# Kernel optimization log

Measured on AMD Instinct MI355X. Metric: run time of the kernel, lower is better.

## Reference

```python
import jax, jax.numpy as jnp
import numpy as np

EPS = 1e-6


def setup_inputs() -> dict:
    key = jax.random.key(0)
    ks = jax.random.split(key, 7)
    b, n, d, H, hid = 4, 512, 128, 4, 32
    scale1 = 1.0 / np.sqrt(2 * d)
    scale2 = 1.0 / np.sqrt(hid)
    return {
        "x": jax.random.normal(ks[0], (b, n, d), dtype=jnp.float32),
        "W1": jax.random.normal(ks[1], (H, 2 * d, hid), dtype=jnp.float32) * scale1,
        "b1": jax.random.normal(ks[2], (H, hid), dtype=jnp.float32) * scale1,
        "W2": jax.random.normal(ks[3], (H, hid), dtype=jnp.float32) * scale2,
        "b2": jax.random.normal(ks[4], (H,), dtype=jnp.float32) * scale2,
        "Wp": jax.random.normal(ks[5], (d, d), dtype=jnp.float32) / np.sqrt(d),
        "bp": jax.random.normal(ks[6], (d,), dtype=jnp.float32) / np.sqrt(d),
    }


def reference(x, W1, b1, W2, b2, Wp, bp):
    # x: [b, n, d]; W1: [H, 2d, hid]; W2: [H, hid]
    d = x.shape[-1]
    # squared pairwise distance via gram matrix: ||xi - xj||^2
    sq = jnp.sum(x * x, axis=-1)                                   # [b, n]
    gram = jnp.einsum("bnd,bmd->bnm", x, x)                        # [b, n, n]
    dist2 = jnp.maximum(sq[:, :, None] + sq[:, None, :] - 2.0 * gram, 0.0)
    # per-head first linear on cat([xi, xj]) split into two projections
    ai = jnp.einsum("bnd,hdk->bhnk", x, W1[:, :d, :])              # [b, H, n, hid]
    aj = jnp.einsum("bnd,hdk->bhnk", x, W1[:, d:, :])              # [b, H, n, hid]
    pre = jnp.tanh(ai[:, :, :, None, :] + aj[:, :, None, :, :]
                   + b1[None, :, None, None, :])                   # [b, H, n, n, hid]
    sigma = jax.nn.softplus(jnp.einsum("bhnmk,hk->bhnm", pre, W2)
                            + b2[None, :, None, None])             # [b, H, n, n]
    adj = jnp.exp(-dist2[:, None, :, :] / (2.0 * sigma * sigma + EPS))
    adj_mean = jnp.mean(adj, axis=1)                               # [b, n, n]
    h = jnp.einsum("bnm,bmd->bnd", adj_mean, x)                    # [b, n, d]
    return h @ Wp + bp
```

## Files before the change

kernel.cpp:

```cpp
#include <hip/hip_runtime.h>

typedef float v4f __attribute__((ext_vector_type(4)));
typedef float v2f __attribute__((ext_vector_type(2)));

#define LOG2E  1.4426950408889634f
#define NLOG2E (-1.4426950408889634f)
#define C2L2E  2.8853900817779268f
#define LN2    0.6931471805599453f

__device__ __forceinline__ float fexp2(float x){ return __builtin_amdgcn_exp2f(x); }
__device__ __forceinline__ float flog2(float x){ return __builtin_amdgcn_logf(x); }
__device__ __forceinline__ float frcp (float x){ return __builtin_amdgcn_rcpf(x); }
__device__ __forceinline__ float hsum(v4f v){ return (v.x+v.y)+(v.z+v.w); }

__global__ __launch_bounds__(256) void prep_kernel(
    const float* __restrict__ x, const float* __restrict__ W1,
    const float* __restrict__ b1, const float* __restrict__ Wp,
    float* __restrict__ sq, float* __restrict__ Abuf,
    float* __restrict__ Bbuf, float* __restrict__ xpT)
{
  const int bid = blockIdx.x, t = threadIdx.x;
  if (bid >= 192) {
    int row = (bid - 192) * 256 + t;
    const v4f* xv = (const v4f*)(x + row * 128);
    float s = 0.f;
#pragma unroll
    for (int q = 0; q < 32; q++) { v4f v = xv[q]; s += hsum(v * v); }
    sq[row] = s;
    return;
  }
  __shared__ v4f Xs[64 * 9];
  __shared__ v4f Ws[32 * 16];
  const bool isAB = bid < 128;
  int it, ct;
  if (isAB) { it = bid >> 2; ct = bid & 3; }
  else      { int q = bid - 128; it = q >> 1; ct = q & 1; }
  const int row0 = it * 64;
  const int tx = t & 15, ty = t >> 4;
  const int r0 = ty * 4, c0 = tx * 4;
  v4f acc[4] = {};

  for (int dd0 = 0; dd0 < 128; dd0 += 32) {
    __syncthreads();
#pragma unroll
    for (int s2 = 0; s2 < 2; s2++) {
      int idx = t + s2 * 256;
      int row = idx >> 3, k4 = idx & 7;
      v4f v = *(const v4f*)(x + (row0 + row) * 128 + dd0 + k4 * 4);
      Xs[row * 9 + ((k4 + (row >> 2)) & 7)] = v;
    }
#pragma unroll
    for (int s2 = 0; s2 < 2; s2++) {
      int idx = t + s2 * 256;
      int dd = idx >> 4, cf4 = idx & 15;
      v4f v;
      if (isAB) {
        int cl = cf4 * 4; int half = cl >> 5; int k = cl & 31;
        v = *(const v4f*)(W1 + (ct * 256 + half * 128 + dd0 + dd) * 32 + k);
      } else {
        v = *(const v4f*)(Wp + (dd0 + dd) * 128 + ct * 64 + cf4 * 4);
      }
      Ws[dd * 16 + cf4] = v;
    }
    __syncthreads();
#pragma unroll
    for (int dd4 = 0; dd4 < 8; dd4++) {
      int sa = (dd4 + ty) & 7;
      v4f a0 = Xs[(r0 + 0) * 9 + sa], a1 = Xs[(r0 + 1) * 9 + sa];
      v4f a2 = Xs[(r0 + 2) * 9 + sa], a3 = Xs[(r0 + 3) * 9 + sa];
#pragma unroll
      for (int u = 0; u < 4; u++) {
        v4f bv = Ws[(dd4 * 4 + u) * 16 + tx];
        acc[0] += a0[u] * bv; acc[1] += a1[u] * bv;
        acc[2] += a2[u] * bv; acc[3] += a3[u] * bv;
      }
    }
  }

  if (isAB) {
    const int h = ct; const int half = c0 >> 5; const int k = c0 & 31;
    v4f bias = {};
    if (half == 0) bias = *(const v4f*)(b1 + h * 32 + k);
    float* dst = (half == 0) ? Abuf : Bbuf;
#pragma unroll
    for (int i = 0; i < 4; i++) {
      int rg = row0 + r0 + i; int b = rg >> 9; int ir = rg & 511;
      v4f o = (acc[i] + bias) * C2L2E;
      *(v4f*)(dst + ((b * 4 + h) * 512 + ir) * 32 + k) = o;
    }
  } else {
    int rg0 = row0 + r0; int b = rg0 >> 9; int ir0 = rg0 & 511;
#pragma unroll
    for (int u = 0; u < 4; u++) {
      int c = ct * 64 + c0 + u;
      v4f o = { acc[0][u], acc[1][u], acc[2][u], acc[3][u] };
      *(v4f*)(xpT + (b * 128 + c) * 512 + ir0) = o;
    }
  }
}

__global__ __launch_bounds__(256) void dist2_kernel(
    const float* __restrict__ x, const float* __restrict__ sq,
    float* __restrict__ D2)
{
  const int jt = blockIdx.x, it = blockIdx.y, b = blockIdx.z;
  const int t = threadIdx.x, tx = t & 15, ty = t >> 4;
  const int r0 = 2 * ty, c0 = 2 * tx;
  __shared__ v4f Xis[32 * 9], Xjs[32 * 9];
  const float* xb = x + b * 512 * 128;
  v4f acc[4] = {};
  const int row = t >> 3, k4l = t & 7, slot = (k4l + (row >> 1)) & 7;

  for (int dd0 = 0; dd0 < 128; dd0 += 32) {
    __syncthreads();
    Xis[row * 9 + slot] = *(const v4f*)(xb + (it * 32 + row) * 128 + dd0 + k4l * 4);
    Xjs[row * 9 + slot] = *(const v4f*)(xb + (jt * 32 + row) * 128 + dd0 + k4l * 4);
    __syncthreads();
#pragma unroll
    for (int k4 = 0; k4 < 8; k4++) {
      int sa = (k4 + ty) & 7, sb = (k4 + tx) & 7;
      v4f a0 = Xis[(r0 + 0) * 9 + sa], a1 = Xis[(r0 + 1) * 9 + sa];
      v4f b0 = Xjs[(c0 + 0) * 9 + sb], b1v = Xjs[(c0 + 1) * 9 + sb];
      acc[0] += a0 * b0; acc[1] += a0 * b1v;
      acc[2] += a1 * b0; acc[3] += a1 * b1v;
    }
  }
  float si0 = sq[b * 512 + it * 32 + r0], si1 = sq[b * 512 + it * 32 + r0 + 1];
  float sj0 = sq[b * 512 + jt * 32 + c0], sj1 = sq[b * 512 + jt * 32 + c0 + 1];
  v2f d0 = { fmaxf(si0 + sj0 - 2.f * hsum(acc[0]), 0.f),
             fmaxf(si0 + sj1 - 2.f * hsum(acc[1]), 0.f) };
  v2f d1 = { fmaxf(si1 + sj0 - 2.f * hsum(acc[2]), 0.f),
             fmaxf(si1 + sj1 - 2.f * hsum(acc[3]), 0.f) };
  float* dst = D2 + ((size_t)(b * 512 + it * 32 + r0)) * 512 + jt * 32 + c0;
  *(v2f*)dst = d0;
  *(v2f*)(dst + 512) = d1;
}

__global__ __launch_bounds__(256) void adj_kernel(
    const float* __restrict__ Abuf, const float* __restrict__ Bbuf,
    const float* __restrict__ W2, const float* __restrict__ b2g,
    const float* __restrict__ D2, float* __restrict__ ADJ)
{
  const int jt = blockIdx.x, it = blockIdx.y, b = blockIdx.z;
  const int t = threadIdx.x, tx = t & 15, ty = t >> 4;
  const int r0 = 2 * ty, c0 = 2 * tx;
  __shared__ v4f As[32 * 9], Bs[32 * 9];
  __shared__ v4f W2s[32];
  __shared__ float hb[4];

  if (t < 32) W2s[t] = ((const v4f*)W2)[t];
  if (t < 4) {
    float s = b2g[t];
    for (int k = 0; k < 32; k++) s += W2[t * 32 + k];
    hb[t] = s;
  }

  const float* d2p = D2 + ((size_t)(b * 512 + it * 32 + r0)) * 512 + jt * 32 + c0;
  v2f d2a = *(const v2f*)d2p;
  v2f d2b = *(const v2f*)(d2p + 512);
  float d2L[4] = { d2a.x * NLOG2E, d2a.y * NLOG2E, d2b.x * NLOG2E, d2b.y * NLOG2E };

  const int row = t >> 3, k4l = t & 7, slot = (k4l + (row >> 1)) & 7;
  float accA[4] = {0.f, 0.f, 0.f, 0.f};

  v4f pa = *(const v4f*)(Abuf + ((size_t)((b * 4 + 0) * 512 + it * 32 + row)) * 32 + k4l * 4);
  v4f pb = *(const v4f*)(Bbuf + ((size_t)((b * 4 + 0) * 512 + jt * 32 + row)) * 32 + k4l * 4);

  for (int h = 0; h < 4; h++) {
    __syncthreads();
    As[row * 9 + slot] = pa;
    Bs[row * 9 + slot] = pb;
    __syncthreads();
    if (h < 3) {
      pa = *(const v4f*)(Abuf + ((size_t)((b * 4 + h + 1) * 512 + it * 32 + row)) * 32 + k4l * 4);
      pb = *(const v4f*)(Bbuf + ((size_t)((b * 4 + h + 1) * 512 + jt * 32 + row)) * 32 + k4l * 4);
    }
    float hbv = hb[h];
    float sacc[4] = { hbv, hbv, hbv, hbv };
#pragma unroll
    for (int k4 = 0; k4 < 8; k4++) {
      int sa = (k4 + ty) & 7, sb = (k4 + tx) & 7;
      v4f a0 = As[(r0 + 0) * 9 + sa], a1 = As[(r0 + 1) * 9 + sa];
      v4f b0 = Bs[(c0 + 0) * 9 + sb], b1v = Bs[(c0 + 1) * 9 + sb];
      v4f w2v = W2s[h * 8 + k4];
#pragma unroll
      for (int u = 0; u < 4; u++) {
        float wm = -2.f * w2v[u];
        float a0u = a0[u], a1u = a1[u], b0u = b0[u], b1u = b1v[u];
        float e;
        e = fexp2(a0u + b0u); sacc[0] = fmaf(wm, frcp(e + 1.f), sacc[0]);
        e = fexp2(a0u + b1u); sacc[1] = fmaf(wm, frcp(e + 1.f), sacc[1]);
        e = fexp2(a1u + b0u); sacc[2] = fmaf(wm, frcp(e + 1.f), sacc[2]);
        e = fexp2(a1u + b1u); sacc[3] = fmaf(wm, frcp(e + 1.f), sacc[3]);
      }
    }
#pragma unroll
    for (int p = 0; p < 4; p++) {
      float u2 = fexp2(sacc[p] * LOG2E);
      float sg = LN2 * flog2(1.f + u2);
      float den = fmaf(2.f * sg, sg, 1e-6f);
      accA[p] += fexp2(d2L[p] * frcp(den));
    }
  }
  float* dst = ADJ + ((size_t)(b * 512 + it * 32 + r0)) * 512 + jt * 32 + c0;
  v2f o0 = { accA[0] * 0.25f, accA[1] * 0.25f };
  v2f o1 = { accA[2] * 0.25f, accA[3] * 0.25f };
  *(v2f*)dst = o0;
  *(v2f*)(dst + 512) = o1;
}

__global__ __launch_bounds__(256) void out_gemm(
    const float* __restrict__ ADJ, const float* __restrict__ xpT,
    float* __restrict__ part)
{
  const int ct = blockIdx.x;
  const int it = blockIdx.y;
  const int z = blockIdx.z; const int b = z >> 2, ks = z & 3;
  const int t = threadIdx.x, tx = t & 15, ty = t >> 4;
  const int r0 = 2 * ty, c0 = 2 * tx;
  __shared__ v4f Ajs[32 * 9], Xps[32 * 9];
  v4f acc[4] = {};
  const int row = t >> 3, k4l = t & 7, slot = (k4l + (row >> 1)) & 7;

  for (int k0 = ks * 128; k0 < ks * 128 + 128; k0 += 32) {
    __syncthreads();
    Ajs[row * 9 + slot] = *(const v4f*)(ADJ + ((size_t)(b * 512 + it * 32 + row)) * 512 + k0 + k4l * 4);
    Xps[row * 9 + slot] = *(const v4f*)(xpT + ((size_t)(b * 128 + ct * 32 + row)) * 512 + k0 + k4l * 4);
    __syncthreads();
#pragma unroll
    for (int k4 = 0; k4 < 8; k4++) {
      int sa = (k4 + ty) & 7, sb = (k4 + tx) & 7;
      v4f a0 = Ajs[(r0 + 0) * 9 + sa], a1 = Ajs[(r0 + 1) * 9 + sa];
      v4f b0 = Xps[(c0 + 0) * 9 + sb], b1v = Xps[(c0 + 1) * 9 + sb];
      acc[0] += a0 * b0; acc[1] += a0 * b1v;
      acc[2] += a1 * b0; acc[3] += a1 * b1v;
    }
  }
  float* dst = part + ((size_t)((ks * 4 + b) * 512 + it * 32 + r0)) * 128 + ct * 32 + c0;
  v2f o0 = { hsum(acc[0]), hsum(acc[1]) };
  v2f o1 = { hsum(acc[2]), hsum(acc[3]) };
  *(v2f*)dst = o0;
  *(v2f*)(dst + 128) = o1;
}

__global__ __launch_bounds__(256) void reduce_out(
    const float* __restrict__ part, const float* __restrict__ bp,
    float* __restrict__ out)
{
  int g = blockIdx.x * 256 + threadIdx.x;
  const v4f* p = (const v4f*)part;
  v4f s = p[g] + p[g + 65536] + p[g + 131072] + p[g + 196608];
  v4f bv = ((const v4f*)bp)[g & 31];
  ((v4f*)out)[g] = s + bv;
}

extern "C" void kernel_launch(void* const* d_in, const int* in_sizes, int n_in,
                              void* d_out, int out_size, void* d_ws, size_t ws_size,
                              hipStream_t stream) {
  const float* x  = (const float*)d_in[0];
  const float* W1 = (const float*)d_in[1];
  const float* b1 = (const float*)d_in[2];
  const float* W2 = (const float*)d_in[3];
  const float* b2 = (const float*)d_in[4];
  const float* Wp = (const float*)d_in[5];
  const float* bp = (const float*)d_in[6];
  float* out = (float*)d_out;

  float* ws  = (float*)d_ws;
  float* sq  = ws;
  float* A   = ws + 2048;
  float* Bb  = A + 262144;
  float* xpT = Bb + 262144;
  float* D2  = xpT + 262144;
  float* ADJ = D2 + 1048576;
  float* part = D2;

  prep_kernel<<<200, 256, 0, stream>>>(x, W1, b1, Wp, sq, A, Bb, xpT);
  dist2_kernel<<<dim3(16, 16, 4), 256, 0, stream>>>(x, sq, D2);
  adj_kernel<<<dim3(16, 16, 4), 256, 0, stream>>>(A, Bb, W2, b2, D2, ADJ);
  out_gemm<<<dim3(4, 16, 16), 256, 0, stream>>>(ADJ, xpT, part);
  reduce_out<<<256, 256, 0, stream>>>(part, bp, out);
}
```

Measured before the change: 68.32 us.

## Fuse distance computation into adjacency kernel and drop split-K output reduction

Moves the Gram-matrix distance computation into the adjacency kernel, reusing its shared-memory tiles, so the D2 matrix is never written to or read back from global memory and one launch disappears. It also replaces the split-K output GEMM plus its separate reduction kernel with a single full-K GEMM that adds the bias directly. This cuts launches and intermediate traffic, but the output GEMM now runs only 256 blocks, each with a four-times-longer K loop, which lowers parallelism.

New measurement: 67.44 us. No clear change (-1.3%).

```diff
diff --git a/kernel.cpp b/kernel.cpp
--- a/kernel.cpp
+++ b/kernel.cpp
@@ -99,47 +99,11 @@
   }
 }
 
-__global__ __launch_bounds__(256) void dist2_kernel(
+__global__ __launch_bounds__(256) void adj_kernel(
     const float* __restrict__ x, const float* __restrict__ sq,
-    float* __restrict__ D2)
-{
-  const int jt = blockIdx.x, it = blockIdx.y, b = blockIdx.z;
-  const int t = threadIdx.x, tx = t & 15, ty = t >> 4;
-  const int r0 = 2 * ty, c0 = 2 * tx;
-  __shared__ v4f Xis[32 * 9], Xjs[32 * 9];
-  const float* xb = x + b * 512 * 128;
-  v4f acc[4] = {};
-  const int row = t >> 3, k4l = t & 7, slot = (k4l + (row >> 1)) & 7;
-
-  for (int dd0 = 0; dd0 < 128; dd0 += 32) {
-    __syncthreads();
-    Xis[row * 9 + slot] = *(const v4f*)(xb + (it * 32 + row) * 128 + dd0 + k4l * 4);
-    Xjs[row * 9 + slot] = *(const v4f*)(xb + (jt * 32 + row) * 128 + dd0 + k4l * 4);
-    __syncthreads();
-#pragma unroll
-    for (int k4 = 0; k4 < 8; k4++) {
-      int sa = (k4 + ty) & 7, sb = (k4 + tx) & 7;
-      v4f a0 = Xis[(r0 + 0) * 9 + sa], a1 = Xis[(r0 + 1) * 9 + sa];
-      v4f b0 = Xjs[(c0 + 0) * 9 + sb], b1v = Xjs[(c0 + 1) * 9 + sb];
-      acc[0] += a0 * b0; acc[1] += a0 * b1v;
-      acc[2] += a1 * b0; acc[3] += a1 * b1v;
-    }
-  }
-  float si0 = sq[b * 512 + it * 32 + r0], si1 = sq[b * 512 + it * 32 + r0 + 1];
-  float sj0 = sq[b * 512 + jt * 32 + c0], sj1 = sq[b * 512 + jt * 32 + c0 + 1];
-  v2f d0 = { fmaxf(si0 + sj0 - 2.f * hsum(acc[0]), 0.f),
-             fmaxf(si0 + sj1 - 2.f * hsum(acc[1]), 0.f) };
-  v2f d1 = { fmaxf(si1 + sj0 - 2.f * hsum(acc[2]), 0.f),
-             fmaxf(si1 + sj1 - 2.f * hsum(acc[3]), 0.f) };
-  float* dst = D2 + ((size_t)(b * 512 + it * 32 + r0)) * 512 + jt * 32 + c0;
-  *(v2f*)dst = d0;
-  *(v2f*)(dst + 512) = d1;
-}
-
-__global__ __launch_bounds__(256) void adj_kernel(
     const float* __restrict__ Abuf, const float* __restrict__ Bbuf,
     const float* __restrict__ W2, const float* __restrict__ b2g,
-    const float* __restrict__ D2, float* __restrict__ ADJ)
+    float* __restrict__ ADJ)
 {
   const int jt = blockIdx.x, it = blockIdx.y, b = blockIdx.z;
   const int t = threadIdx.x, tx = t & 15, ty = t >> 4;
@@ -155,17 +119,36 @@
     hb[t] = s;
   }
 
-  const float* d2p = D2 + ((size_t)(b * 512 + it * 32 + r0)) * 512 + jt * 32 + c0;
-  v2f d2a = *(const v2f*)d2p;
-  v2f d2b = *(const v2f*)(d2p + 512);
-  float d2L[4] = { d2a.x * NLOG2E, d2a.y * NLOG2E, d2b.x * NLOG2E, d2b.y * NLOG2E };
-
   const int row = t >> 3, k4l = t & 7, slot = (k4l + (row >> 1)) & 7;
-  float accA[4] = {0.f, 0.f, 0.f, 0.f};
+  const float* xb = x + b * 512 * 128;
 
   v4f pa = *(const v4f*)(Abuf + ((size_t)((b * 4 + 0) * 512 + it * 32 + row)) * 32 + k4l * 4);
   v4f pb = *(const v4f*)(Bbuf + ((size_t)((b * 4 + 0) * 512 + jt * 32 + row)) * 32 + k4l * 4);
 
+  v4f gacc[4] = {};
+  for (int dd0 = 0; dd0 < 128; dd0 += 32) {
+    __syncthreads();
+    As[row * 9 + slot] = *(const v4f*)(xb + (it * 32 + row) * 128 + dd0 + k4l * 4);
+    Bs[row * 9 + slot] = *(const v4f*)(xb + (jt * 32 + row) * 128 + dd0 + k4l * 4);
+    __syncthreads();
+#pragma unroll
+    for (int k4 = 0; k4 < 8; k4++) {
+      int sa = (k4 + ty) & 7, sb = (k4 + tx) & 7;
+      v4f a0 = As[(r0 + 0) * 9 + sa], a1 = As[(r0 + 1) * 9 + sa];
+      v4f b0 = Bs[(c0 + 0) * 9 + sb], b1v = Bs[(c0 + 1) * 9 + sb];
+      gacc[0] += a0 * b0; gacc[1] += a0 * b1v;
+      gacc[2] += a1 * b0; gacc[3] += a1 * b1v;
+    }
+  }
+  float si0 = sq[b * 512 + it * 32 + r0], si1 = sq[b * 512 + it * 32 + r0 + 1];
+  float sj0 = sq[b * 512 + jt * 32 + c0], sj1 = sq[b * 512 + jt * 32 + c0 + 1];
+  float d2L[4] = {
+    fmaxf(si0 + sj0 - 2.f * hsum(gacc[0]), 0.f) * NLOG2E,
+    fmaxf(si0 + sj1 - 2.f * hsum(gacc[1]), 0.f) * NLOG2E,
+    fmaxf(si1 + sj0 - 2.f * hsum(gacc[2]), 0.f) * NLOG2E,
+    fmaxf(si1 + sj1 - 2.f * hsum(gacc[3]), 0.f) * NLOG2E };
+
+  float accA[4] = {0.f, 0.f, 0.f, 0.f};
   for (int h = 0; h < 4; h++) {
     __syncthreads();
     As[row * 9 + slot] = pa;
@@ -209,20 +192,20 @@
   *(v2f*)(dst + 512) = o1;
 }
 
-__global__ __launch_bounds__(256) void out_gemm(
+__global__ __launch_bounds__(256) void out_kernel(
     const float* __restrict__ ADJ, const float* __restrict__ xpT,
-    float* __restrict__ part)
+    const float* __restrict__ bp, float* __restrict__ out)
 {
   const int ct = blockIdx.x;
   const int it = blockIdx.y;
-  const int z = blockIdx.z; const int b = z >> 2, ks = z & 3;
+  const int b = blockIdx.z;
   const int t = threadIdx.x, tx = t & 15, ty = t >> 4;
   const int r0 = 2 * ty, c0 = 2 * tx;
   __shared__ v4f Ajs[32 * 9], Xps[32 * 9];
   v4f acc[4] = {};
   const int row = t >> 3, k4l = t & 7, slot = (k4l + (row >> 1)) & 7;
 
-  for (int k0 = ks * 128; k0 < ks * 128 + 128; k0 += 32) {
+  for (int k0 = 0; k0 < 512; k0 += 32) {
     __syncthreads();
     Ajs[row * 9 + slot] = *(const v4f*)(ADJ + ((size_t)(b * 512 + it * 32 + row)) * 512 + k0 + k4l * 4);
     Xps[row * 9 + slot] = *(const v4f*)(xpT + ((size_t)(b * 128 + ct * 32 + row)) * 512 + k0 + k4l * 4);
@@ -236,22 +219,12 @@
       acc[2] += a1 * b0; acc[3] += a1 * b1v;
     }
   }
-  float* dst = part + ((size_t)((ks * 4 + b) * 512 + it * 32 + r0)) * 128 + ct * 32 + c0;
-  v2f o0 = { hsum(acc[0]), hsum(acc[1]) };
-  v2f o1 = { hsum(acc[2]), hsum(acc[3]) };
+  float bp0 = bp[ct * 32 + c0], bp1 = bp[ct * 32 + c0 + 1];
+  float* dst = out + ((size_t)(b * 512 + it * 32 + r0)) * 128 + ct * 32 + c0;
+  v2f o0 = { hsum(acc[0]) + bp0, hsum(acc[1]) + bp1 };
+  v2f o1 = { hsum(acc[2]) + bp0, hsum(acc[3]) + bp1 };
   *(v2f*)dst = o0;
   *(v2f*)(dst + 128) = o1;
-}
-
-__global__ __launch_bounds__(256) void reduce_out(
-    const float* __restrict__ part, const float* __restrict__ bp,
-    float* __restrict__ out)
-{
-  int g = blockIdx.x * 256 + threadIdx.x;
-  const v4f* p = (const v4f*)part;
-  v4f s = p[g] + p[g + 65536] + p[g + 131072] + p[g + 196608];
-  v4f bv = ((const v4f*)bp)[g & 31];
-  ((v4f*)out)[g] = s + bv;
 }
 
 extern "C" void kernel_launch(void* const* d_in, const int* in_sizes, int n_in,
@@ -271,13 +244,9 @@
   float* A   = ws + 2048;
   float* Bb  = A + 262144;
   float* xpT = Bb + 262144;
-  float* D2  = xpT + 262144;
-  float* ADJ = D2 + 1048576;
-  float* part = D2;
+  float* ADJ = xpT + 262144;
 
   prep_kernel<<<200, 256, 0, stream>>>(x, W1, b1, Wp, sq, A, Bb, xpT);
-  dist2_kernel<<<dim3(16, 16, 4), 256, 0, stream>>>(x, sq, D2);
-  adj_kernel<<<dim3(16, 16, 4), 256, 0, stream>>>(A, Bb, W2, b2, D2, ADJ);
-  out_gemm<<<dim3(4, 16, 16), 256, 0, stream>>>(ADJ, xpT, part);
-  reduce_out<<<256, 256, 0, stream>>>(part, bp, out);
-}
+  adj_kernel<<<dim3(16, 16, 4), 256, 0, stream>>>(x, sq, A, Bb, W2, b2, ADJ);
+  out_kernel<<<dim3(4, 16, 4), 256, 0, stream>>>(ADJ, xpT, bp, out);
+}
```
